# Performance work log

Measured on AMD Instinct MI355X. Metric: run time of the kernel, lower is better.

The kernel has to match this reference:

```python
import jax, jax.numpy as jnp
import numpy as np
import math

H, W = 1024, 1280
NUM_CLASSES = 81  # 80 foreground + background
CENTER_VAR, SIZE_VAR = 0.1, 0.2
CONF_THR, NMS_THR = 0.01, 0.45
PRE_NMS_K, MAX_DET = 400, 100

def make_priors():
    strides_x = [32, 64, 128, 213, 320]
    strides_y = [32, 64, 128, 256, 512]
    fmx = [int(W / s) for s in strides_x]
    fmy = [int(H / s) for s in strides_y]
    expand = H / 256.0
    mins = [10 * expand, 62 * expand, 114 * expand, 166 * expand, 218 * expand]
    maxs = [62 * expand, 114 * expand, 166 * expand, 218 * expand, 270 * expand]
    ars = [[2, 3], [2, 3], [2, 3], [2], [2]]
    pri = []
    for k in range(5):
        for i in range(fmy[k]):
            for j in range(fmx[k]):
                cx = (j + 0.5) / fmx[k]
                cy = (i + 0.5) / fmy[k]
                pri.append([cx, cy, mins[k] / W, mins[k] / H])
                s = math.sqrt(mins[k] * maxs[k])
                pri.append([cx, cy, s / W, s / H])
                for r in ars[k]:
                    sr = math.sqrt(r)
                    pri.append([cx, cy, mins[k] * sr / W, mins[k] / sr / H])
                    pri.append([cx, cy, mins[k] / sr / W, mins[k] * sr / H])
    return np.clip(np.asarray(pri, np.float32), 0.0, 1.0)  # [P,4] center form

def setup_inputs():
    key = jax.random.key(0)
    k1, k2 = jax.random.split(key)
    pri = jnp.asarray(make_priors())  # [10208, 4]
    P = pri.shape[0]
    return {
        "cls_logits": jax.random.normal(k1, (32, P, NUM_CLASSES), jnp.float32),
        "bbox_pred": jax.random.normal(k2, (32, P, 4), jnp.float32) * 0.5,
        "priors": pri,
    }

def _decode(loc, priors):
    # convert_locations_to_boxes: center-form decode with variances
    c = loc[..., :2] * CENTER_VAR * priors[..., 2:] + priors[..., :2]
    s = jnp.exp(loc[..., 2:] * SIZE_VAR) * priors[..., 2:]
    # center_form_to_corner_form
    return jnp.concatenate([c - s * 0.5, c + s * 0.5], axis=-1)

def _iou(a, b):
    lt = jnp.maximum(a[:, None, :2], b[None, :, :2])
    rb = jnp.minimum(a[:, None, 2:], b[None, :, 2:])
    wh = jnp.clip(rb - lt, 0.0)
    inter = wh[..., 0] * wh[..., 1]
    ar = (a[:, 2] - a[:, 0]) * (a[:, 3] - a[:, 1])
    br = (b[:, 2] - b[:, 0]) * (b[:, 3] - b[:, 1])
    return inter / (ar[:, None] + br[None, :] - inter + 1e-9)

def _post_one(scores, boxes):
    # scores: [P, C] softmax probs, boxes: [P, 4] corner form in [0,1]
    C = scores.shape[1]
    fg = scores[:, 1:]  # drop background
    bx = boxes * jnp.asarray([W, H, W, H], boxes.dtype)  # scale to image coords
    topv, topi = jax.lax.top_k(fg.reshape(-1), PRE_NMS_K)  # pre-NMS candidates
    prior_idx = topi // (C - 1)
    cls = topi % (C - 1) + 1
    cb = bx[prior_idx]  # [K,4]
    # class-aware (batched) NMS: offset boxes by class so classes never overlap
    off = cls.astype(bx.dtype)[:, None] * float(max(H, W) + 1)
    ob = cb + off
    iou = _iou(ob, ob)  # [K,K]
    keep0 = topv > CONF_THR
    idx = jnp.arange(PRE_NMS_K)
    def body(keep, i):
        sup = (iou[i] > NMS_THR) & (idx > i) & keep[i]
        return keep & ~sup, None
    keep, _ = jax.lax.scan(body, keep0, jnp.arange(PRE_NMS_K))
    sc = jnp.where(keep, topv, 0.0)
    fv, fi = jax.lax.top_k(sc, MAX_DET)
    return cb[fi], cls[fi], fv  # boxes [100,4], labels [100], scores [100]

def reference(cls_logits, bbox_pred, priors):
    scores = jax.nn.softmax(cls_logits, axis=2)  # [B,P,C]
    boxes = _decode(bbox_pred, priors)           # [B,P,4]
    return jax.vmap(_post_one)(scores, boxes)
```

## Files before the change

kernel.cpp:

```cpp
#include <hip/hip_runtime.h>


#define BATCH   32
#define NCLS    81
#define CM1     80
#define KPRE    400
#define MAXDET  100
#define NBINS   4096
#define CAP     32768
#define THRESH  0.06f
#define CONFT   0.01f
#define NMST    0.45f
#define OFFMUL  1281.0f
#define WD      1280.0f
#define HT      1024.0f

#define SPB     256

#define OFF_CNT   0u
#define ZERO_BYTES 256u
#define OFF_CAND  1024u
#define OFF_TOPV  8389632u
#define OFF_CLS   8440832u
#define OFF_BOX   8492032u
#define OFF_SUP   8696832u

__device__ __forceinline__ int binof(unsigned int bits) {
    int e = (int)(bits >> 23);
    int k = (e - 122) * 512 + (int)((bits >> 14) & 0x1FF);
    return max(0, min(k, NBINS - 1));
}

__global__ __launch_bounds__(256, 3) void k_score(const float* __restrict__ logits,
                                                  unsigned int* __restrict__ cnt,
                                                  uint2* __restrict__ cand, int P) {
    int b = blockIdx.y;
    int p0 = blockIdx.x * SPB;
    int npb = min(SPB, P - p0);
    int t = threadIdx.x;
    __shared__ unsigned int blk_cnt, blk_base;

    if (t == 0) blk_cnt = 0;
    __syncthreads();

    bool active = (t < npb);
    float x[NCLS];
    float mx = 0.f, s = 0.f, thr = 0.f;
    unsigned int mycnt = 0, myoff = 0;
    if (active) {
        const float* __restrict__ row = logits + ((size_t)b * P + p0 + t) * NCLS;
        #pragma unroll
        for (int c = 0; c < NCLS; ++c) x[c] = row[c];

        float m0 = x[0], m1 = x[1], m2 = x[2], m3 = x[3];
        #pragma unroll
        for (int c = 4; c + 3 < NCLS; c += 4) {
            m0 = fmaxf(m0, x[c]);     m1 = fmaxf(m1, x[c + 1]);
            m2 = fmaxf(m2, x[c + 2]); m3 = fmaxf(m3, x[c + 3]);
        }
        mx = fmaxf(fmaxf(fmaxf(m0, m1), fmaxf(m2, m3)), x[NCLS - 1]);
        s = 0.0f;
        #pragma unroll
        for (int c = 0; c < NCLS; ++c) s = __fadd_rn(s, expf(__fsub_rn(x[c], mx)));
        thr = mx + logf(THRESH * s) - 1e-3f;
        #pragma unroll
        for (int c = 1; c < NCLS; ++c) mycnt += (x[c] > thr) ? 1u : 0u;
        if (mycnt) myoff = atomicAdd(&blk_cnt, mycnt);
    }
    __syncthreads();
    if (t == 0) blk_base = atomicAdd(&cnt[b], blk_cnt);
    __syncthreads();

    if (active && mycnt) {
        unsigned int pos = blk_base + myoff;
        unsigned int baseIdx = (unsigned int)(p0 + t) * CM1;
        #pragma unroll
        for (int c = 1; c < NCLS; ++c) {
            float xv = x[c];
            if (xv > thr) {
                float pr = __fdiv_rn(expf(__fsub_rn(xv, mx)), s);
                if (pos < CAP)
                    cand[(size_t)b * CAP + pos] = make_uint2(__float_as_uint(pr),
                                                             baseIdx + (unsigned)(c - 1));
                pos++;
            }
        }
    }
}

__global__ __launch_bounds__(512) void k_select(const unsigned int* __restrict__ cnt,
                                                const uint2* __restrict__ cand,
                                                const float* __restrict__ bbox,
                                                const float* __restrict__ priors,
                                                float* __restrict__ topv,
                                                unsigned int* __restrict__ clsA,
                                                float* __restrict__ boxA, int P) {
    int b = blockIdx.x;
    int tid = threadIdx.x;
    __shared__ unsigned int lh[NBINS];
    __shared__ unsigned long long keys[2048];
    __shared__ unsigned int sh_bstar, sh_M;

    for (int i = tid; i < NBINS; i += 512) lh[i] = 0u;
    if (tid == 0) sh_M = 0;
    __syncthreads();

    unsigned int n = min(cnt[b], (unsigned)CAP);
    const uint2* cb = cand + (size_t)b * CAP;
    {
        unsigned int j = tid;
        for (; j + 1536 < n; j += 2048) {
            uint2 c0 = cb[j], c1 = cb[j + 512], c2 = cb[j + 1024], c3 = cb[j + 1536];
            atomicAdd(&lh[binof(c0.x)], 1u);
            atomicAdd(&lh[binof(c1.x)], 1u);
            atomicAdd(&lh[binof(c2.x)], 1u);
            atomicAdd(&lh[binof(c3.x)], 1u);
        }
        for (; j < n; j += 512) atomicAdd(&lh[binof(cb[j].x)], 1u);
    }
    __syncthreads();

    if (tid < 64) {
        int lane = tid;
        unsigned int bsum = 0;
        for (int m = 0; m < 64; ++m) { int mm = (m + lane) & 63; bsum += lh[lane * 64 + mm]; }
        unsigned int S = bsum;
        for (int off = 1; off < 64; off <<= 1) {
            unsigned int o = __shfl(S, min(lane + off, 63));
            if (lane + off < 64) S += o;
        }
        unsigned int Sn = __shfl(S, min(lane + 1, 63)); if (lane == 63) Sn = 0;
        bool cond = (S >= KPRE) && (Sn < KPRE);
        unsigned long long bal = __ballot(cond);
        int Ls = (bal == 0) ? 0 : (__ffsll((long long)bal) - 1);
        unsigned int coarse = __shfl(Sn, Ls);
        unsigned int T = lh[Ls * 64 + lane];
        for (int off = 1; off < 64; off <<= 1) {
            unsigned int o = __shfl(T, min(lane + off, 63));
            if (lane + off < 64) T += o;
        }
        unsigned int Tn = __shfl(T, min(lane + 1, 63)); if (lane == 63) Tn = 0;
        bool cond2 = (coarse + T >= KPRE) && (coarse + Tn < KPRE);
        unsigned long long bal2 = __ballot(cond2);
        int Ms = (bal2 == 0) ? 0 : (__ffsll((long long)bal2) - 1);
        if (lane == 0) sh_bstar = (unsigned)(Ls * 64 + Ms);
    }
    __syncthreads();
    int bstar = (int)sh_bstar;

    {
        unsigned int j = tid;
        for (; j + 1536 < n; j += 2048) {
            uint2 c0 = cb[j], c1 = cb[j + 512], c2 = cb[j + 1024], c3 = cb[j + 1536];
            if (binof(c0.x) >= bstar) {
                unsigned int pos = atomicAdd(&sh_M, 1u);
                if (pos < 2048) keys[pos] = ((unsigned long long)c0.x << 32) | (unsigned int)(~c0.y);
            }
            if (binof(c1.x) >= bstar) {
                unsigned int pos = atomicAdd(&sh_M, 1u);
                if (pos < 2048) keys[pos] = ((unsigned long long)c1.x << 32) | (unsigned int)(~c1.y);
            }
            if (binof(c2.x) >= bstar) {
                unsigned int pos = atomicAdd(&sh_M, 1u);
                if (pos < 2048) keys[pos] = ((unsigned long long)c2.x << 32) | (unsigned int)(~c2.y);
            }
            if (binof(c3.x) >= bstar) {
                unsigned int pos = atomicAdd(&sh_M, 1u);
                if (pos < 2048) keys[pos] = ((unsigned long long)c3.x << 32) | (unsigned int)(~c3.y);
            }
        }
        for (; j < n; j += 512) {
            uint2 cd = cb[j];
            if (binof(cd.x) >= bstar) {
                unsigned int pos = atomicAdd(&sh_M, 1u);
                if (pos < 2048) keys[pos] = ((unsigned long long)cd.x << 32) | (unsigned int)(~cd.y);
            }
        }
    }
    __syncthreads();
    unsigned int M = min(sh_M, 2048u);
    unsigned int S2 = 512; while (S2 < M) S2 <<= 1;
    for (unsigned int i = M + tid; i < S2; i += 512) keys[i] = 0ull;
    __syncthreads();

    for (unsigned int k = 2; k <= S2; k <<= 1) {
        for (unsigned int j = k >> 1; j > 0; j >>= 1) {
            for (unsigned int i = tid; i < S2; i += 512) {
                unsigned int pi = i ^ j;
                if (pi > i) {
                    unsigned long long a = keys[i], bb = keys[pi];
                    bool sw = ((i & k) == 0) ? (a < bb) : (a > bb);
                    if (sw) { keys[i] = bb; keys[pi] = a; }
                }
            }
            __syncthreads();
        }
    }

    for (int k2 = tid; k2 < KPRE; k2 += 512) {
        unsigned long long key = keys[k2];
        unsigned int bits = (unsigned int)(key >> 32);
        unsigned int idx = ~((unsigned int)key);
        float val, x1, y1, x2, y2; unsigned int cc;
        if (bits == 0u) { val = 0.f; x1 = y1 = x2 = y2 = 0.f; cc = 0u; }
        else {
            val = __uint_as_float(bits);
            unsigned int prior = idx / CM1;
            cc = idx - prior * CM1 + 1u;
            const float* lp = bbox + ((size_t)b * P + prior) * 4;
            const float* pp = priors + (size_t)prior * 4;
            float cx = __fadd_rn(__fmul_rn(__fmul_rn(lp[0], 0.1f), pp[2]), pp[0]);
            float cy = __fadd_rn(__fmul_rn(__fmul_rn(lp[1], 0.1f), pp[3]), pp[1]);
            float sw = __fmul_rn(expf(__fmul_rn(lp[2], 0.2f)), pp[2]);
            float sh = __fmul_rn(expf(__fmul_rn(lp[3], 0.2f)), pp[3]);
            x1 = __fmul_rn(__fsub_rn(cx, __fmul_rn(sw, 0.5f)), WD);
            y1 = __fmul_rn(__fsub_rn(cy, __fmul_rn(sh, 0.5f)), HT);
            x2 = __fmul_rn(__fadd_rn(cx, __fmul_rn(sw, 0.5f)), WD);
            y2 = __fmul_rn(__fadd_rn(cy, __fmul_rn(sh, 0.5f)), HT);
        }
        size_t o = (size_t)b * KPRE + k2;
        topv[o] = val; clsA[o] = cc;
        boxA[o * 4 + 0] = x1; boxA[o * 4 + 1] = y1; boxA[o * 4 + 2] = x2; boxA[o * 4 + 3] = y2;
    }
}

__global__ __launch_bounds__(512) void k_iou(const float* __restrict__ boxA,
                                             const unsigned int* __restrict__ clsA,
                                             unsigned long long* __restrict__ sup) {
    int b = blockIdx.x;
    int w = blockIdx.y;
    int tid = threadIdx.x;
    __shared__ float ob[KPRE][4];
    const float4* box4 = (const float4*)boxA;
    for (int k = tid; k < KPRE; k += 512) {
        size_t o = (size_t)b * KPRE + k;
        float4 bx = box4[o];
        float off = __fmul_rn((float)clsA[o], OFFMUL);
        ob[k][0] = __fadd_rn(bx.x, off);
        ob[k][1] = __fadd_rn(bx.y, off);
        ob[k][2] = __fadd_rn(bx.z, off);
        ob[k][3] = __fadd_rn(bx.w, off);
    }
    __syncthreads();
    int i = tid;
    if (i >= KPRE) return;
    float a0 = ob[i][0], a1 = ob[i][1], a2 = ob[i][2], a3 = ob[i][3];
    float ar = __fmul_rn(__fsub_rn(a2, a0), __fsub_rn(a3, a1));
    unsigned long long m = 0ull;
    int jmax = min(64, KPRE - w * 64);
    for (int jb = 0; jb < jmax; ++jb) {
        int j = w * 64 + jb;
        float ltx = fmaxf(a0, ob[j][0]), lty = fmaxf(a1, ob[j][1]);
        float rbx = fminf(a2, ob[j][2]), rby = fminf(a3, ob[j][3]);
        float wd = fmaxf(__fsub_rn(rbx, ltx), 0.0f);
        float ht = fmaxf(__fsub_rn(rby, lty), 0.0f);
        float inter = __fmul_rn(wd, ht);
        float br = __fmul_rn(__fsub_rn(ob[j][2], ob[j][0]), __fsub_rn(ob[j][3], ob[j][1]));
        float den = __fadd_rn(__fsub_rn(__fadd_rn(ar, br), inter), 1e-9f);
        float iou = __fdiv_rn(inter, den);
        if (j > i && iou > NMST) m |= (1ull << jb);
    }
    sup[((size_t)b * KPRE + i) * 7 + w] = m;
}

__global__ __launch_bounds__(128) void k_nms(const unsigned long long* __restrict__ sup,
                                             const float* __restrict__ topv,
                                             const unsigned int* __restrict__ clsA,
                                             const float* __restrict__ boxA,
                                             float* __restrict__ out) {
    int b = blockIdx.x;
    int tid = threadIdx.x;
    __shared__ unsigned long long ls[KPRE * 7];
    __shared__ float tv[KPRE];
    __shared__ unsigned long long keepw[7];
    for (int w = tid; w < KPRE * 7; w += 128) ls[w] = sup[(size_t)b * KPRE * 7 + w];
    for (int k = tid; k < KPRE; k += 128) tv[k] = topv[(size_t)b * KPRE + k];
    if (tid < 7) keepw[tid] = 0ull;
    __syncthreads();
    for (int k = tid; k < KPRE; k += 128)
        if (tv[k] > CONFT) atomicOr(&keepw[k >> 6], 1ull << (k & 63));
    __syncthreads();

    if (tid < 64) {
        unsigned long long q0 = keepw[0], q1 = keepw[1], q2 = keepw[2], q3 = keepw[3],
                           q4 = keepw[4], q5 = keepw[5], q6 = keepw[6];
        unsigned long long rb[4][7];
        #pragma unroll
        for (int d = 0; d < 4; ++d) {
            #pragma unroll
            for (int w2 = 0; w2 < 7; ++w2) rb[d][w2] = ls[(unsigned)(d * 7 + w2)];
        }
#define SCANW(W, QW, NB)                                                          \
        for (int b4 = 0; b4 < NB; b4 += 4) {                                      \
            _Pragma("unroll")                                                     \
            for (int u = 0; u < 4; ++u) {                                         \
                int k = W * 64 + b4 + u;                                          \
                unsigned long long msk =                                          \
                    ((QW >> (b4 + u)) & 1ull) ? ~0ull : 0ull;                     \
                q0 &= ~(rb[u][0] & msk); q1 &= ~(rb[u][1] & msk);                 \
                q2 &= ~(rb[u][2] & msk); q3 &= ~(rb[u][3] & msk);                 \
                q4 &= ~(rb[u][4] & msk); q5 &= ~(rb[u][5] & msk);                 \
                q6 &= ~(rb[u][6] & msk);                                          \
                if (k + 4 < KPRE) {                                               \
                    _Pragma("unroll")                                             \
                    for (int w2 = 0; w2 < 7; ++w2)                                \
                        rb[u][w2] = ls[(unsigned)((k + 4) * 7 + w2)];             \
                }                                                                 \
            }                                                                     \
        }
        SCANW(0, q0, 64) SCANW(1, q1, 64) SCANW(2, q2, 64) SCANW(3, q3, 64)
        SCANW(4, q4, 64) SCANW(5, q5, 64) SCANW(6, q6, 16)
#undef SCANW
        if (tid == 0) {
            keepw[0] = q0; keepw[1] = q1; keepw[2] = q2; keepw[3] = q3;
            keepw[4] = q4; keepw[5] = q5; keepw[6] = q6;
        }
    }
    __syncthreads();

    int tot = 0;
    for (int t = 0; t < 7; ++t) tot += __popcll(keepw[t]);
    for (int k = tid; k < KPRE; k += 128) {
        int w = k >> 6, bi = k & 63;
        unsigned long long kw = keepw[w];
        int before = __popcll(kw & ((1ull << bi) - 1ull));
        for (int t = 0; t < w; ++t) before += __popcll(keepw[t]);
        bool kept = (kw >> bi) & 1ull;
        int rank = kept ? before : (tot + (k - before));
        if (rank < MAXDET) {
            size_t so = (size_t)b * KPRE + k;
            size_t dof = (size_t)b * MAXDET + rank;
            out[dof * 4 + 0] = boxA[so * 4 + 0];
            out[dof * 4 + 1] = boxA[so * 4 + 1];
            out[dof * 4 + 2] = boxA[so * 4 + 2];
            out[dof * 4 + 3] = boxA[so * 4 + 3];
            out[(size_t)BATCH * MAXDET * 4 + dof] = (float)clsA[so];
            out[(size_t)BATCH * MAXDET * 5 + dof] = kept ? tv[k] : 0.0f;
        }
    }
}

extern "C" void kernel_launch(void* const* d_in, const int* in_sizes, int n_in,
                              void* d_out, int out_size, void* d_ws, size_t ws_size,
                              hipStream_t stream) {
    (void)n_in; (void)out_size; (void)ws_size;
    const float* logits = (const float*)d_in[0];
    const float* bbox   = (const float*)d_in[1];
    const float* priors = (const float*)d_in[2];
    int P = in_sizes[2] / 4;

    char* ws = (char*)d_ws;
    unsigned int* cnt  = (unsigned int*)(ws + OFF_CNT);
    uint2* cand        = (uint2*)(ws + OFF_CAND);
    float* topv        = (float*)(ws + OFF_TOPV);
    unsigned int* clsA = (unsigned int*)(ws + OFF_CLS);
    float* boxA        = (float*)(ws + OFF_BOX);
    unsigned long long* sup = (unsigned long long*)(ws + OFF_SUP);

    hipMemsetAsync(ws, 0, ZERO_BYTES, stream);

    dim3 g1((P + SPB - 1) / SPB, BATCH);
    k_score<<<g1, 256, 0, stream>>>(logits, cnt, cand, P);
    k_select<<<BATCH, 512, 0, stream>>>(cnt, cand, bbox, priors, topv, clsA, boxA, P);
    k_iou<<<dim3(BATCH, 7), 512, 0, stream>>>(boxA, clsA, sup);
    k_nms<<<BATCH, 128, 0, stream>>>(sup, topv, clsA, boxA, (float*)d_out);
}
```

Measured before the change: 266.7 us.

## Fuse select, IoU, and NMS kernels into one per-batch kernel

Merges the top-K selection, the pairwise IoU suppression-mask build and the greedy NMS scan into a single kernel per image. Boxes, scores, classes and the suppression masks stay in shared memory, which removes three global round trips and two kernel launches. In exchange the IoU work, formerly spread across 7×32 blocks, now runs in only 32 blocks with one thread per candidate doing all 400 comparisons. Shared memory use also rises to about 70KB per block.

```diff
diff --git a/kernel.cpp b/kernel.cpp
--- a/kernel.cpp
+++ b/kernel.cpp
@@ -20,10 +20,6 @@
 #define OFF_CNT   0u
 #define ZERO_BYTES 256u
 #define OFF_CAND  1024u
-#define OFF_TOPV  8389632u
-#define OFF_CLS   8440832u
-#define OFF_BOX   8492032u
-#define OFF_SUP   8696832u
 
 __device__ __forceinline__ int binof(unsigned int bits) {
     int e = (int)(bits >> 23);
@@ -88,21 +84,26 @@
     }
 }
 
-__global__ __launch_bounds__(512) void k_select(const unsigned int* __restrict__ cnt,
-                                                const uint2* __restrict__ cand,
-                                                const float* __restrict__ bbox,
-                                                const float* __restrict__ priors,
-                                                float* __restrict__ topv,
-                                                unsigned int* __restrict__ clsA,
-                                                float* __restrict__ boxA, int P) {
+__global__ __launch_bounds__(512) void k_fused(const unsigned int* __restrict__ cnt,
+                                               const uint2* __restrict__ cand,
+                                               const float* __restrict__ bbox,
+                                               const float* __restrict__ priors,
+                                               float* __restrict__ out, int P) {
     int b = blockIdx.x;
     int tid = threadIdx.x;
     __shared__ unsigned int lh[NBINS];
     __shared__ unsigned long long keys[2048];
     __shared__ unsigned int sh_bstar, sh_M;
+    __shared__ float bxr[KPRE][4];
+    __shared__ float ob[KPRE][4];
+    __shared__ float tv[KPRE];
+    __shared__ unsigned int clsS[KPRE];
+    __shared__ unsigned long long ls[KPRE * 7];
+    __shared__ unsigned long long keepw[7];
 
     for (int i = tid; i < NBINS; i += 512) lh[i] = 0u;
     if (tid == 0) sh_M = 0;
+    if (tid < 7) keepw[tid] = 0ull;
     __syncthreads();
 
     unsigned int n = min(cnt[b], (unsigned)CAP);
@@ -197,8 +198,9 @@
         }
     }
 
-    for (int k2 = tid; k2 < KPRE; k2 += 512) {
-        unsigned long long key = keys[k2];
+    float a0 = 0.f, a1 = 0.f, a2 = 0.f, a3 = 0.f;
+    if (tid < KPRE) {
+        unsigned long long key = keys[tid];
         unsigned int bits = (unsigned int)(key >> 32);
         unsigned int idx = ~((unsigned int)key);
         float val, x1, y1, x2, y2; unsigned int cc;
@@ -218,77 +220,61 @@
             x2 = __fmul_rn(__fadd_rn(cx, __fmul_rn(sw, 0.5f)), WD);
             y2 = __fmul_rn(__fadd_rn(cy, __fmul_rn(sh, 0.5f)), HT);
         }
-        size_t o = (size_t)b * KPRE + k2;
-        topv[o] = val; clsA[o] = cc;
-        boxA[o * 4 + 0] = x1; boxA[o * 4 + 1] = y1; boxA[o * 4 + 2] = x2; boxA[o * 4 + 3] = y2;
-    }
-}
-
-__global__ __launch_bounds__(512) void k_iou(const float* __restrict__ boxA,
-                                             const unsigned int* __restrict__ clsA,
-                                             unsigned long long* __restrict__ sup) {
-    int b = blockIdx.x;
-    int w = blockIdx.y;
-    int tid = threadIdx.x;
-    __shared__ float ob[KPRE][4];
-    const float4* box4 = (const float4*)boxA;
-    for (int k = tid; k < KPRE; k += 512) {
-        size_t o = (size_t)b * KPRE + k;
-        float4 bx = box4[o];
-        float off = __fmul_rn((float)clsA[o], OFFMUL);
-        ob[k][0] = __fadd_rn(bx.x, off);
-        ob[k][1] = __fadd_rn(bx.y, off);
-        ob[k][2] = __fadd_rn(bx.z, off);
-        ob[k][3] = __fadd_rn(bx.w, off);
-    }
-    __syncthreads();
-    int i = tid;
-    if (i >= KPRE) return;
-    float a0 = ob[i][0], a1 = ob[i][1], a2 = ob[i][2], a3 = ob[i][3];
-    float ar = __fmul_rn(__fsub_rn(a2, a0), __fsub_rn(a3, a1));
-    unsigned long long m = 0ull;
-    int jmax = min(64, KPRE - w * 64);
-    for (int jb = 0; jb < jmax; ++jb) {
-        int j = w * 64 + jb;
-        float ltx = fmaxf(a0, ob[j][0]), lty = fmaxf(a1, ob[j][1]);
-        float rbx = fminf(a2, ob[j][2]), rby = fminf(a3, ob[j][3]);
-        float wd = fmaxf(__fsub_rn(rbx, ltx), 0.0f);
-        float ht = fmaxf(__fsub_rn(rby, lty), 0.0f);
-        float inter = __fmul_rn(wd, ht);
-        float br = __fmul_rn(__fsub_rn(ob[j][2], ob[j][0]), __fsub_rn(ob[j][3], ob[j][1]));
-        float den = __fadd_rn(__fsub_rn(__fadd_rn(ar, br), inter), 1e-9f);
-        float iou = __fdiv_rn(inter, den);
-        if (j > i && iou > NMST) m |= (1ull << jb);
-    }
-    sup[((size_t)b * KPRE + i) * 7 + w] = m;
-}
-
-__global__ __launch_bounds__(128) void k_nms(const unsigned long long* __restrict__ sup,
-                                             const float* __restrict__ topv,
-                                             const unsigned int* __restrict__ clsA,
-                                             const float* __restrict__ boxA,
-                                             float* __restrict__ out) {
-    int b = blockIdx.x;
-    int tid = threadIdx.x;
-    __shared__ unsigned long long ls[KPRE * 7];
-    __shared__ float tv[KPRE];
-    __shared__ unsigned long long keepw[7];
-    for (int w = tid; w < KPRE * 7; w += 128) ls[w] = sup[(size_t)b * KPRE * 7 + w];
-    for (int k = tid; k < KPRE; k += 128) tv[k] = topv[(size_t)b * KPRE + k];
-    if (tid < 7) keepw[tid] = 0ull;
-    __syncthreads();
-    for (int k = tid; k < KPRE; k += 128)
-        if (tv[k] > CONFT) atomicOr(&keepw[k >> 6], 1ull << (k & 63));
+        tv[tid] = val; clsS[tid] = cc;
+        bxr[tid][0] = x1; bxr[tid][1] = y1; bxr[tid][2] = x2; bxr[tid][3] = y2;
+        float off = __fmul_rn((float)cc, OFFMUL);
+        a0 = __fadd_rn(x1, off); a1 = __fadd_rn(y1, off);
+        a2 = __fadd_rn(x2, off); a3 = __fadd_rn(y2, off);
+        ob[tid][0] = a0; ob[tid][1] = a1; ob[tid][2] = a2; ob[tid][3] = a3;
+    }
+    __syncthreads();
+
+    if (tid < KPRE) {
+        int i = tid;
+        float ar = __fmul_rn(__fsub_rn(a2, a0), __fsub_rn(a3, a1));
+        const float4* ob4 = (const float4*)ob;
+        float4 rb[4];
+        #pragma unroll
+        for (int u = 0; u < 4; ++u) rb[u] = ob4[u];
+#define IOUW(W, NB)                                                               \
+        {                                                                         \
+            unsigned long long m = 0ull;                                          \
+            for (int jb = 0; jb < NB; jb += 4) {                                  \
+                _Pragma("unroll")                                                 \
+                for (int u = 0; u < 4; ++u) {                                     \
+                    int j = W * 64 + jb + u;                                      \
+                    float4 bx = rb[u];                                            \
+                    float ltx = fmaxf(a0, bx.x), lty = fmaxf(a1, bx.y);           \
+                    float rbx_ = fminf(a2, bx.z), rby_ = fminf(a3, bx.w);         \
+                    float wd = fmaxf(__fsub_rn(rbx_, ltx), 0.0f);                 \
+                    float ht = fmaxf(__fsub_rn(rby_, lty), 0.0f);                 \
+                    float inter = __fmul_rn(wd, ht);                              \
+                    float br = __fmul_rn(__fsub_rn(bx.z, bx.x),                   \
+                                         __fsub_rn(bx.w, bx.y));                  \
+                    float den = __fadd_rn(__fsub_rn(__fadd_rn(ar, br), inter),    \
+                                          1e-9f);                                 \
+                    float iou = __fdiv_rn(inter, den);                            \
+                    if (j > i && iou > NMST) m |= (1ull << (jb + u));             \
+                    if (j + 4 < KPRE) rb[u] = ob4[j + 4];                         \
+                }                                                                 \
+            }                                                                     \
+            ls[(unsigned)i * 7u + (unsigned)W] = m;                               \
+        }
+        IOUW(0, 64) IOUW(1, 64) IOUW(2, 64) IOUW(3, 64)
+        IOUW(4, 64) IOUW(5, 64) IOUW(6, 16)
+#undef IOUW
+        if (tv[tid] > CONFT) atomicOr(&keepw[tid >> 6], 1ull << (tid & 63));
+    }
     __syncthreads();
 
     if (tid < 64) {
         unsigned long long q0 = keepw[0], q1 = keepw[1], q2 = keepw[2], q3 = keepw[3],
                            q4 = keepw[4], q5 = keepw[5], q6 = keepw[6];
-        unsigned long long rb[4][7];
+        unsigned long long rbm[4][7];
         #pragma unroll
         for (int d = 0; d < 4; ++d) {
             #pragma unroll
-            for (int w2 = 0; w2 < 7; ++w2) rb[d][w2] = ls[(unsigned)(d * 7 + w2)];
+            for (int w2 = 0; w2 < 7; ++w2) rbm[d][w2] = ls[(unsigned)(d * 7 + w2)];
         }
 #define SCANW(W, QW, NB)                                                          \
         for (int b4 = 0; b4 < NB; b4 += 4) {                                      \
@@ -297,14 +283,14 @@
                 int k = W * 64 + b4 + u;                                          \
                 unsigned long long msk =                                          \
                     ((QW >> (b4 + u)) & 1ull) ? ~0ull : 0ull;                     \
-                q0 &= ~(rb[u][0] & msk); q1 &= ~(rb[u][1] & msk);                 \
-                q2 &= ~(rb[u][2] & msk); q3 &= ~(rb[u][3] & msk);                 \
-                q4 &= ~(rb[u][4] & msk); q5 &= ~(rb[u][5] & msk);                 \
-                q6 &= ~(rb[u][6] & msk);                                          \
+                q0 &= ~(rbm[u][0] & msk); q1 &= ~(rbm[u][1] & msk);               \
+                q2 &= ~(rbm[u][2] & msk); q3 &= ~(rbm[u][3] & msk);               \
+                q4 &= ~(rbm[u][4] & msk); q5 &= ~(rbm[u][5] & msk);               \
+                q6 &= ~(rbm[u][6] & msk);                                         \
                 if (k + 4 < KPRE) {                                               \
                     _Pragma("unroll")                                             \
                     for (int w2 = 0; w2 < 7; ++w2)                                \
-                        rb[u][w2] = ls[(unsigned)((k + 4) * 7 + w2)];             \
+                        rbm[u][w2] = ls[(unsigned)((k + 4) * 7 + w2)];            \
                 }                                                                 \
             }                                                                     \
         }
@@ -319,22 +305,22 @@
     __syncthreads();
 
     int tot = 0;
-    for (int t = 0; t < 7; ++t) tot += __popcll(keepw[t]);
-    for (int k = tid; k < KPRE; k += 128) {
-        int w = k >> 6, bi = k & 63;
-        unsigned long long kw = keepw[w];
+    for (int t2 = 0; t2 < 7; ++t2) tot += __popcll(keepw[t2]);
+    if (tid < KPRE) {
+        int k = tid;
+        int w2 = k >> 6, bi = k & 63;
+        unsigned long long kw = keepw[w2];
         int before = __popcll(kw & ((1ull << bi) - 1ull));
-        for (int t = 0; t < w; ++t) before += __popcll(keepw[t]);
+        for (int t2 = 0; t2 < w2; ++t2) before += __popcll(keepw[t2]);
         bool kept = (kw >> bi) & 1ull;
         int rank = kept ? before : (tot + (k - before));
         if (rank < MAXDET) {
-            size_t so = (size_t)b * KPRE + k;
             size_t dof = (size_t)b * MAXDET + rank;
-            out[dof * 4 + 0] = boxA[so * 4 + 0];
-            out[dof * 4 + 1] = boxA[so * 4 + 1];
-            out[dof * 4 + 2] = boxA[so * 4 + 2];
-            out[dof * 4 + 3] = boxA[so * 4 + 3];
-            out[(size_t)BATCH * MAXDET * 4 + dof] = (float)clsA[so];
+            out[dof * 4 + 0] = bxr[k][0];
+            out[dof * 4 + 1] = bxr[k][1];
+            out[dof * 4 + 2] = bxr[k][2];
+            out[dof * 4 + 3] = bxr[k][3];
+            out[(size_t)BATCH * MAXDET * 4 + dof] = (float)clsS[k];
             out[(size_t)BATCH * MAXDET * 5 + dof] = kept ? tv[k] : 0.0f;
         }
     }
@@ -352,16 +338,10 @@
     char* ws = (char*)d_ws;
     unsigned int* cnt  = (unsigned int*)(ws + OFF_CNT);
     uint2* cand        = (uint2*)(ws + OFF_CAND);
-    float* topv        = (float*)(ws + OFF_TOPV);
-    unsigned int* clsA = (unsigned int*)(ws + OFF_CLS);
-    float* boxA        = (float*)(ws + OFF_BOX);
-    unsigned long long* sup = (unsigned long long*)(ws + OFF_SUP);
 
     hipMemsetAsync(ws, 0, ZERO_BYTES, stream);
 
     dim3 g1((P + SPB - 1) / SPB, BATCH);
     k_score<<<g1, 256, 0, stream>>>(logits, cnt, cand, P);
-    k_select<<<BATCH, 512, 0, stream>>>(cnt, cand, bbox, priors, topv, clsA, boxA, P);
-    k_iou<<<dim3(BATCH, 7), 512, 0, stream>>>(boxA, clsA, sup);
-    k_nms<<<BATCH, 128, 0, stream>>>(sup, topv, clsA, boxA, (float*)d_out);
+    k_fused<<<BATCH, 512, 0, stream>>>(cnt, cand, bbox, priors, (float*)d_out, P);
 }
```

Result: slower. 296.5 us (+11.2%).

## Build per-batch score histogram in k_score via global atomics

Applied to the files above, without the earlier changes.

The score kernel now atomically increments a per-batch global histogram for each candidate it emits. The select kernel then loads that histogram instead of re-reading all candidates to build one in shared memory. This removes a full pass over the candidate buffer in the select kernel, which runs only 32 blocks. In exchange it adds global atomics with heavy contention in the score kernel and an extra memset. The histogram aliases the suppression-mask region, which k_iou writes later.

```diff
diff --git a/kernel.cpp b/kernel.cpp
--- a/kernel.cpp
+++ b/kernel.cpp
@@ -24,6 +24,8 @@
 #define OFF_CLS   8440832u
 #define OFF_BOX   8492032u
 #define OFF_SUP   8696832u
+#define OFF_HIST  OFF_SUP
+#define HIST_BYTES (BATCH * NBINS * 4u)
 
 __device__ __forceinline__ int binof(unsigned int bits) {
     int e = (int)(bits >> 23);
@@ -33,6 +35,7 @@
 
 __global__ __launch_bounds__(256, 3) void k_score(const float* __restrict__ logits,
                                                   unsigned int* __restrict__ cnt,
+                                                  unsigned int* __restrict__ ghist,
                                                   uint2* __restrict__ cand, int P) {
     int b = blockIdx.y;
     int p0 = blockIdx.x * SPB;
@@ -74,14 +77,18 @@
     if (active && mycnt) {
         unsigned int pos = blk_base + myoff;
         unsigned int baseIdx = (unsigned int)(p0 + t) * CM1;
+        unsigned int* hb = ghist + ((unsigned)b << 12);
         #pragma unroll
         for (int c = 1; c < NCLS; ++c) {
             float xv = x[c];
             if (xv > thr) {
                 float pr = __fdiv_rn(expf(__fsub_rn(xv, mx)), s);
-                if (pos < CAP)
-                    cand[(size_t)b * CAP + pos] = make_uint2(__float_as_uint(pr),
+                if (pos < CAP) {
+                    unsigned int bits = __float_as_uint(pr);
+                    cand[(size_t)b * CAP + pos] = make_uint2(bits,
                                                              baseIdx + (unsigned)(c - 1));
+                    atomicAdd(&hb[binof(bits)], 1u);
+                }
                 pos++;
             }
         }
@@ -89,6 +96,7 @@
 }
 
 __global__ __launch_bounds__(512) void k_select(const unsigned int* __restrict__ cnt,
+                                                const unsigned int* __restrict__ ghist,
                                                 const uint2* __restrict__ cand,
                                                 const float* __restrict__ bbox,
                                                 const float* __restrict__ priors,
@@ -101,23 +109,9 @@
     __shared__ unsigned long long keys[2048];
     __shared__ unsigned int sh_bstar, sh_M;
 
-    for (int i = tid; i < NBINS; i += 512) lh[i] = 0u;
+    const unsigned int* hb = ghist + ((unsigned)b << 12);
+    for (int i = tid; i < NBINS; i += 512) lh[i] = hb[i];
     if (tid == 0) sh_M = 0;
-    __syncthreads();
-
-    unsigned int n = min(cnt[b], (unsigned)CAP);
-    const uint2* cb = cand + (size_t)b * CAP;
-    {
-        unsigned int j = tid;
-        for (; j + 1536 < n; j += 2048) {
-            uint2 c0 = cb[j], c1 = cb[j + 512], c2 = cb[j + 1024], c3 = cb[j + 1536];
-            atomicAdd(&lh[binof(c0.x)], 1u);
-            atomicAdd(&lh[binof(c1.x)], 1u);
-            atomicAdd(&lh[binof(c2.x)], 1u);
-            atomicAdd(&lh[binof(c3.x)], 1u);
-        }
-        for (; j < n; j += 512) atomicAdd(&lh[binof(cb[j].x)], 1u);
-    }
     __syncthreads();
 
     if (tid < 64) {
@@ -148,6 +142,8 @@
     __syncthreads();
     int bstar = (int)sh_bstar;
 
+    unsigned int n = min(cnt[b], (unsigned)CAP);
+    const uint2* cb = cand + (size_t)b * CAP;
     {
         unsigned int j = tid;
         for (; j + 1536 < n; j += 2048) {
@@ -350,18 +346,20 @@
     int P = in_sizes[2] / 4;
 
     char* ws = (char*)d_ws;
-    unsigned int* cnt  = (unsigned int*)(ws + OFF_CNT);
-    uint2* cand        = (uint2*)(ws + OFF_CAND);
-    float* topv        = (float*)(ws + OFF_TOPV);
-    unsigned int* clsA = (unsigned int*)(ws + OFF_CLS);
-    float* boxA        = (float*)(ws + OFF_BOX);
+    unsigned int* cnt   = (unsigned int*)(ws + OFF_CNT);
+    unsigned int* ghist = (unsigned int*)(ws + OFF_HIST);
+    uint2* cand         = (uint2*)(ws + OFF_CAND);
+    float* topv         = (float*)(ws + OFF_TOPV);
+    unsigned int* clsA  = (unsigned int*)(ws + OFF_CLS);
+    float* boxA         = (float*)(ws + OFF_BOX);
     unsigned long long* sup = (unsigned long long*)(ws + OFF_SUP);
 
     hipMemsetAsync(ws, 0, ZERO_BYTES, stream);
+    hipMemsetAsync(ws + OFF_HIST, 0, HIST_BYTES, stream);
 
     dim3 g1((P + SPB - 1) / SPB, BATCH);
-    k_score<<<g1, 256, 0, stream>>>(logits, cnt, cand, P);
-    k_select<<<BATCH, 512, 0, stream>>>(cnt, cand, bbox, priors, topv, clsA, boxA, P);
+    k_score<<<g1, 256, 0, stream>>>(logits, cnt, ghist, cand, P);
+    k_select<<<BATCH, 512, 0, stream>>>(cnt, ghist, cand, bbox, priors, topv, clsA, boxA, P);
     k_iou<<<dim3(BATCH, 7), 512, 0, stream>>>(boxA, clsA, sup);
     k_nms<<<BATCH, 128, 0, stream>>>(sup, topv, clsA, boxA, (float*)d_out);
 }
```

Measured after the change: 314.7 us. +18.0%, slower.
